# Performance work log

Hardware: AMD Instinct MI355X
Metric: run time of the kernel (lower is better)

The kernel has to match this reference:

```python
import jax, jax.numpy as jnp
import numpy as np

B, T, D, H = 4, 2048, 1024, 16
DH = D // H          # 64
HALF = DH // 2       # 32


def _rope_tables(T, half, base=10000.0):
    inv_freq = 1.0 / (base ** (np.arange(half, dtype=np.float32) / half))
    t = np.arange(T, dtype=np.float32)
    ang = np.outer(t, inv_freq)                       # [T, half]
    cos = jnp.asarray(np.cos(ang))[None, None]        # [1,1,T,half]
    sin = jnp.asarray(np.sin(ang))[None, None]
    return cos, sin


def setup_inputs() -> dict:
    key = jax.random.key(0)
    kx, kq, kp = jax.random.split(key, 3)
    cos, sin = _rope_tables(T, HALF)
    return {
        "x": jax.random.normal(kx, (B, T, D), dtype=jnp.float32),
        "cos": cos,
        "sin": sin,
        "W_qkv": jax.random.normal(kq, (3 * D, D), dtype=jnp.float32) * (D ** -0.5),
        "W_proj": jax.random.normal(kp, (D, D), dtype=jnp.float32) * (D ** -0.5),
    }


def _apply_rope(q, k, cos, sin):
    # q,k: [B,H,T,dh]; cos,sin: [1,1,T,dh/2]
    t = q.shape[2]
    c, s = cos[:, :, :t, :], sin[:, :, :t, :]
    h = q.shape[-1] // 2
    q1, q2 = q[..., :h], q[..., h:]
    k1, k2 = k[..., :h], k[..., h:]
    q_rot = jnp.concatenate([q1 * c - q2 * s, q1 * s + q2 * c], axis=-1)
    k_rot = jnp.concatenate([k1 * c - k2 * s, k1 * s + k2 * c], axis=-1)
    return q_rot, k_rot


def reference(x, cos, sin, W_qkv, W_proj):
    Bb, Tt, C = x.shape
    qkv = x @ W_qkv.T                                 # [B,T,3C]
    q, k, v = jnp.split(qkv, 3, axis=2)
    # [B,T,C] -> [B,H,T,dh]
    q = q.reshape(Bb, Tt, H, DH).transpose(0, 2, 1, 3)
    k = k.reshape(Bb, Tt, H, DH).transpose(0, 2, 1, 3)
    v = v.reshape(Bb, Tt, H, DH).transpose(0, 2, 1, 3)
    q, k = _apply_rope(q, k, cos, sin)
    w = jnp.einsum("bhqd,bhkd->bhqk", q, k) * (DH ** -0.5)
    causal = jnp.tril(jnp.ones((Tt, Tt), dtype=bool))
    w = jnp.where(causal, w, -jnp.inf)
    w = jax.nn.softmax(w.astype(jnp.float32), axis=-1).astype(x.dtype)
    out = jnp.einsum("bhqk,bhkd->bhqd", w, v)
    # XSA: subtract self-value contribution (diagonal attention weight)
    self_w = jnp.diagonal(w, axis1=-2, axis2=-1)[..., None]  # [B,H,T,1]
    out = out - self_w * v
    out = out.transpose(0, 2, 1, 3).reshape(Bb, Tt, C)
    return out @ W_proj.T
```

## Files before the change

kernel.cpp:

```cpp
#include <hip/hip_runtime.h>

constexpr int Tq = 2048;
constexpr int Dq = 1024;

typedef __bf16 bf16x8 __attribute__((ext_vector_type(8)));
typedef float f32x4 __attribute__((ext_vector_type(4)));
typedef _Float16 f16;
typedef f16 f16x4 __attribute__((ext_vector_type(4)));
typedef unsigned short u16;
typedef u16 u16x4 __attribute__((ext_vector_type(4)));
typedef u16 u16x8 __attribute__((ext_vector_type(8)));

__device__ __forceinline__ u16 f2bf(float f) {
    unsigned int u = __float_as_uint(f);
    u += 0x7fffu + ((u >> 16) & 1u);
    return (u16)(u >> 16);
}

__device__ __forceinline__ void gld_lds16(const void* g, void* l) {
    __builtin_amdgcn_global_load_lds(
        (const __attribute__((address_space(1))) unsigned int*)g,
        (__attribute__((address_space(3))) unsigned int*)l, 16, 0, 0);
}

__global__ void cvt3_f32_bf16(const float* __restrict__ a, u16* __restrict__ oa, int na,
                              const float* __restrict__ b, u16* __restrict__ ob, int nb,
                              const float* __restrict__ c, u16* __restrict__ oc, int nc) {
    int i = blockIdx.x * 256 + threadIdx.x;
    const float* in; u16* out;
    if (i < na) { in = a; out = oa; }
    else if (i < na + nb) { in = b; out = ob; i -= na; }
    else if (i < na + nb + nc) { in = c; out = oc; i -= na + nb; }
    else return;
    float4 v = ((const float4*)in)[i];
    u16x4 o;
    o.x = f2bf(v.x); o.y = f2bf(v.y); o.z = f2bf(v.z); o.w = f2bf(v.w);
    ((u16x4*)out)[i] = o;
}

__global__ __launch_bounds__(256) void gemm_qkv(const u16* __restrict__ A,
                                                const u16* __restrict__ B,
                                                const float* __restrict__ cosT,
                                                const float* __restrict__ sinT,
                                                u16* __restrict__ Qb,
                                                u16* __restrict__ Kb,
                                                f16* __restrict__ Vtg) {
    constexpr int K = 1024, N = 3072;
    __shared__ u16 As[128 * 32];
    __shared__ u16 Bs[128 * 32];
    const int t = threadIdx.x;
    const int lane = t & 63;
    const int wave = t >> 6;
    const int l16 = lane & 15;
    const int quad = lane >> 4;
    const int bm = blockIdx.x * 128;
    const int by = blockIdx.y;
    const int bn = by * 128;
    const int wm = (wave & 1) * 64;
    const int wn = (wave >> 1) * 64;
    const int srow = t >> 2;
    const int scol = (t & 3) * 8;

    f32x4 acc[4][4] = {};

    const u16* Ab = A + (size_t)(bm + srow) * K + scol;
    const u16* Bb = B + (size_t)(bn + srow) * K + scol;

    for (int k0 = 0; k0 < K; k0 += 32) {
        gld_lds16(Ab + k0,                    (char*)As + t * 16);
        gld_lds16(Ab + (size_t)64 * K + k0,   (char*)As + 4096 + t * 16);
        gld_lds16(Bb + k0,                    (char*)Bs + t * 16);
        gld_lds16(Bb + (size_t)64 * K + k0,   (char*)Bs + 4096 + t * 16);
        __syncthreads();

        bf16x8 af[4], bf[4];
#pragma unroll
        for (int i = 0; i < 4; i++) {
            af[i] = *(const bf16x8*)&As[(wm + i * 16 + l16) * 32 + quad * 8];
            bf[i] = *(const bf16x8*)&Bs[(wn + i * 16 + l16) * 32 + quad * 8];
        }
#pragma unroll
        for (int i = 0; i < 4; i++)
#pragma unroll
            for (int j = 0; j < 4; j++)
                acc[i][j] = __builtin_amdgcn_mfma_f32_16x16x32_bf16(af[i], bf[j], acc[i][j], 0, 0, 0);
        __syncthreads();
    }

    const int kind = by >> 3;
    if (kind < 2) {
        u16* Out = kind ? Kb : Qb;
        const float qscale = kind ? 1.f : 0.18033688011112042f;
        const int h = ((by & 7) << 1) + (wn >> 6);
#pragma unroll
        for (int i = 0; i < 4; i++)
#pragma unroll
            for (int r = 0; r < 4; r++) {
                const int gm = bm + wm + i * 16 + quad * 4 + r;
                const int b = gm >> 11, tt = gm & 2047;
                const size_t row = ((size_t)(b * 16 + h) * Tq + tt) * 64;
#pragma unroll
                for (int jj = 0; jj < 2; jj++) {
                    const int dd = jj * 16 + l16;
                    const float c = cosT[tt * 32 + dd];
                    const float s = sinT[tt * 32 + dd];
                    const float v1 = acc[i][jj][r];
                    const float v2 = acc[i][jj + 2][r];
                    Out[row + dd]      = f2bf((v1 * c - v2 * s) * qscale);
                    Out[row + dd + 32] = f2bf((v1 * s + v2 * c) * qscale);
                }
            }
    } else {
#pragma unroll
        for (int i = 0; i < 4; i++) {
            const int gm0 = bm + wm + i * 16 + quad * 4;
            const int b = gm0 >> 11, tt = gm0 & 2047;
#pragma unroll
            for (int j = 0; j < 4; j++) {
                const int col = wn + j * 16 + l16;
                const int h = ((by & 7) << 1) + (col >> 6);
                const int d = col & 63;
                f16x4 o = {(f16)acc[i][j][0], (f16)acc[i][j][1],
                           (f16)acc[i][j][2], (f16)acc[i][j][3]};
                *(f16x4*)&Vtg[((size_t)(b * 16 + h) * 64 + d) * Tq + tt] = o;
            }
        }
    }
}

__global__ __launch_bounds__(256) void gemm_bt(const u16* __restrict__ A,
                                               const u16* __restrict__ B,
                                               float* __restrict__ Cv,
                                               int M, int N, int K) {
    __shared__ u16 As[128 * 32];
    __shared__ u16 Bs[128 * 32];
    const int t = threadIdx.x;
    const int lane = t & 63;
    const int wave = t >> 6;
    const int l16 = lane & 15;
    const int quad = lane >> 4;
    const int bm = blockIdx.x * 128;
    const int bn = blockIdx.y * 128;
    const int wm = (wave & 1) * 64;
    const int wn = (wave >> 1) * 64;
    const int srow = t >> 2;
    const int scol = (t & 3) * 8;

    f32x4 acc[4][4] = {};

    const u16* Ab = A + (size_t)(bm + srow) * K + scol;
    const u16* Bb = B + (size_t)(bn + srow) * K + scol;

    for (int k0 = 0; k0 < K; k0 += 32) {
        gld_lds16(Ab + k0,                    (char*)As + t * 16);
        gld_lds16(Ab + (size_t)64 * K + k0,   (char*)As + 4096 + t * 16);
        gld_lds16(Bb + k0,                    (char*)Bs + t * 16);
        gld_lds16(Bb + (size_t)64 * K + k0,   (char*)Bs + 4096 + t * 16);
        __syncthreads();

        bf16x8 af[4], bf[4];
#pragma unroll
        for (int i = 0; i < 4; i++) {
            af[i] = *(const bf16x8*)&As[(wm + i * 16 + l16) * 32 + quad * 8];
            bf[i] = *(const bf16x8*)&Bs[(wn + i * 16 + l16) * 32 + quad * 8];
        }
#pragma unroll
        for (int i = 0; i < 4; i++)
#pragma unroll
            for (int j = 0; j < 4; j++)
                acc[i][j] = __builtin_amdgcn_mfma_f32_16x16x32_bf16(af[i], bf[j], acc[i][j], 0, 0, 0);
        __syncthreads();
    }

#pragma unroll
    for (int i = 0; i < 4; i++)
#pragma unroll
        for (int j = 0; j < 4; j++)
#pragma unroll
            for (int r = 0; r < 4; r++) {
                const int gm = bm + wm + i * 16 + quad * 4 + r;
                const int gn = bn + wn + j * 16 + l16;
                Cv[(size_t)gm * N + gn] = acc[i][j][r];
            }
}

template <bool MASK>
__device__ __forceinline__ void flash_tile(const u16* __restrict__ Ks,
                                           const f16* __restrict__ Vs,
                                           const bf16x8& qf0, const bf16x8& qf1,
                                           int l16, int quad, int i_loc,
                                           float& l_run, f32x4* o_acc) {
    f32x4 s[4];
    const int cp0 = quad ^ (l16 & 7);
    const int cp1 = (4 + quad) ^ (l16 & 7);
    __builtin_amdgcn_s_setprio(1);
#pragma unroll
    for (int tn = 0; tn < 4; tn++) {
        const int jrow = tn * 16 + l16;
        bf16x8 kf0 = *(const bf16x8*)&Ks[jrow * 64 + cp0 * 8];
        bf16x8 kf1 = *(const bf16x8*)&Ks[jrow * 64 + cp1 * 8];
        f32x4 z = {0.f, 0.f, 0.f, 0.f};
        z = __builtin_amdgcn_mfma_f32_16x16x32_bf16(kf0, qf0, z, 0, 0, 0);
        z = __builtin_amdgcn_mfma_f32_16x16x32_bf16(kf1, qf1, z, 0, 0, 0);
        s[tn] = z;
    }
    __builtin_amdgcn_s_setprio(0);
    float rsa[4];
#pragma unroll
    for (int tn = 0; tn < 4; tn++) {
        float rs = 0.f;
#pragma unroll
        for (int r = 0; r < 4; r++) {
            float v = s[tn][r];
            if (MASK) {
                const int j_loc = tn * 16 + quad * 4 + r;
                if (j_loc > i_loc) v = -1e30f;
            }
            float p = exp2f(v);
            rs += p;
            if (MASK) {
                const int j_loc = tn * 16 + quad * 4 + r;
                if (j_loc == i_loc) p = 0.f;
            }
            s[tn][r] = p;
        }
        rsa[tn] = rs;
    }
    l_run += (rsa[0] + rsa[1]) + (rsa[2] + rsa[3]);

    f16x4 pf[4];
#pragma unroll
    for (int tk = 0; tk < 4; tk++)
        pf[tk] = f16x4{(f16)s[tk][0], (f16)s[tk][1], (f16)s[tk][2], (f16)s[tk][3]};
    __builtin_amdgcn_s_setprio(1);
#pragma unroll
    for (int td = 0; td < 4; td++) {
        const int drow = td * 16 + l16;
#pragma unroll
        for (int tk = 0; tk < 4; tk++) {
            const int cp = (2 * tk + (quad >> 1)) ^ (l16 & 7);
            f16x4 vf = *(const f16x4*)&Vs[drow * 64 + cp * 8 + (quad & 1) * 4];
            o_acc[td] = __builtin_amdgcn_mfma_f32_16x16x16f16(vf, pf[tk], o_acc[td], 0, 0, 0);
        }
    }
    __builtin_amdgcn_s_setprio(0);
}

template <bool MASKA>
__device__ __forceinline__ void flash_tile2(const u16* __restrict__ Ks,
                                            const f16* __restrict__ Vs,
                                            const bf16x8& qa0, const bf16x8& qa1,
                                            const bf16x8& qb0, const bf16x8& qb1,
                                            int l16, int quad, int i_loc,
                                            float& lA, f32x4* oA,
                                            float& lB, f32x4* oB) {
    f32x4 sA[4], sB[4];
    const int cp0 = quad ^ (l16 & 7);
    const int cp1 = (4 + quad) ^ (l16 & 7);
    __builtin_amdgcn_s_setprio(1);
#pragma unroll
    for (int tn = 0; tn < 4; tn++) {
        const int jrow = tn * 16 + l16;
        bf16x8 kf0 = *(const bf16x8*)&Ks[jrow * 64 + cp0 * 8];
        bf16x8 kf1 = *(const bf16x8*)&Ks[jrow * 64 + cp1 * 8];
        f32x4 zA = {0.f, 0.f, 0.f, 0.f}, zB = {0.f, 0.f, 0.f, 0.f};
        zA = __builtin_amdgcn_mfma_f32_16x16x32_bf16(kf0, qa0, zA, 0, 0, 0);
        zB = __builtin_amdgcn_mfma_f32_16x16x32_bf16(kf0, qb0, zB, 0, 0, 0);
        zA = __builtin_amdgcn_mfma_f32_16x16x32_bf16(kf1, qa1, zA, 0, 0, 0);
        zB = __builtin_amdgcn_mfma_f32_16x16x32_bf16(kf1, qb1, zB, 0, 0, 0);
        sA[tn] = zA; sB[tn] = zB;
    }
    __builtin_amdgcn_s_setprio(0);
    float raA = 0.f, raB = 0.f;
#pragma unroll
    for (int tn = 0; tn < 4; tn++) {
#pragma unroll
        for (int r = 0; r < 4; r++) {
            float vA = sA[tn][r];
            if (MASKA) {
                const int j_loc = tn * 16 + quad * 4 + r;
                if (j_loc > i_loc) vA = -1e30f;
            }
            float pA = exp2f(vA);
            raA += pA;
            if (MASKA) {
                const int j_loc = tn * 16 + quad * 4 + r;
                if (j_loc == i_loc) pA = 0.f;
            }
            sA[tn][r] = pA;
            float pB = exp2f(sB[tn][r]);
            raB += pB;
            sB[tn][r] = pB;
        }
    }
    lA += raA; lB += raB;

    f16x4 pfA[4], pfB[4];
#pragma unroll
    for (int tk = 0; tk < 4; tk++) {
        pfA[tk] = f16x4{(f16)sA[tk][0], (f16)sA[tk][1], (f16)sA[tk][2], (f16)sA[tk][3]};
        pfB[tk] = f16x4{(f16)sB[tk][0], (f16)sB[tk][1], (f16)sB[tk][2], (f16)sB[tk][3]};
    }
    __builtin_amdgcn_s_setprio(1);
#pragma unroll
    for (int td = 0; td < 4; td++) {
        const int drow = td * 16 + l16;
#pragma unroll
        for (int tk = 0; tk < 4; tk++) {
            const int cp = (2 * tk + (quad >> 1)) ^ (l16 & 7);
            f16x4 vf = *(const f16x4*)&Vs[drow * 64 + cp * 8 + (quad & 1) * 4];
            oA[td] = __builtin_amdgcn_mfma_f32_16x16x16f16(vf, pfA[tk], oA[td], 0, 0, 0);
            oB[td] = __builtin_amdgcn_mfma_f32_16x16x16f16(vf, pfB[tk], oB[td], 0, 0, 0);
        }
    }
    __builtin_amdgcn_s_setprio(0);
}

__global__ __launch_bounds__(256, 2) void flash(const u16* __restrict__ Qb,
                                                const u16* __restrict__ Kb,
                                                const f16* __restrict__ Vtg,
                                                u16* __restrict__ Ob) {
    __shared__ __align__(16) char smem[65536];

    const int t = threadIdx.x, lane = t & 63, wave = t >> 6;
    const int l16 = lane & 15, quad = lane >> 4;
    const int i = blockIdx.x;
    const int xcd = i & 7, w = i >> 3;
    const int bh = xcd * 8 + (w >> 4);
    const int b = bh >> 4, h = bh & 15;
    const int x = w & 15;
    const int qtA = x, qtB = 31 - x;
    const int q0a = qtA * 64, q0b = qtB * 64;
    const u16* Qp = Qb + (size_t)bh * Tq * 64;
    const u16* Kp = Kb + (size_t)bh * Tq * 64;
    const f16* Vp = Vtg + (size_t)bh * 64 * Tq;

    const int rowi = wave * 16 + l16;
    bf16x8 qa0 = *(const bf16x8*)(Qp + (size_t)(q0a + rowi) * 64 + quad * 8);
    bf16x8 qa1 = *(const bf16x8*)(Qp + (size_t)(q0a + rowi) * 64 + 32 + quad * 8);
    bf16x8 qb0 = *(const bf16x8*)(Qp + (size_t)(q0b + rowi) * 64 + quad * 8);
    bf16x8 qb1 = *(const bf16x8*)(Qp + (size_t)(q0b + rowi) * 64 + 32 + quad * 8);
    asm volatile("s_waitcnt vmcnt(0)"
                 : "+v"(qa0), "+v"(qa1), "+v"(qb0), "+v"(qb1) :: "memory");

    float lA = 0.f, lB = 0.f;
    f32x4 oA[4] = {}, oB[4] = {};

    const int sr = t >> 3;
    const int sc = (t & 7) ^ (sr & 7);
    const int i_tloc = wave * 16 + l16;
    const int nt = 32 - x;
    const int nt2 = (nt + 1) >> 1;

    auto stage = [&](int n2) {
        const int j0 = n2 * 128;
        char* buf = smem + (n2 & 1) * 32768;
        gld_lds16(Kp + (size_t)(j0 + sr) * 64 + sc * 8,            buf + t * 16);
        gld_lds16(Kp + (size_t)(j0 + 32 + sr) * 64 + sc * 8,       buf + 4096 + t * 16);
        gld_lds16(Kp + (size_t)(j0 + 64 + sr) * 64 + sc * 8,       buf + 8192 + t * 16);
        gld_lds16(Kp + (size_t)(j0 + 96 + sr) * 64 + sc * 8,       buf + 12288 + t * 16);
        gld_lds16(Vp + (size_t)sr * Tq + j0 + sc * 8,              buf + 16384 + t * 16);
        gld_lds16(Vp + (size_t)(32 + sr) * Tq + j0 + sc * 8,       buf + 20480 + t * 16);
        gld_lds16(Vp + (size_t)sr * Tq + j0 + 64 + sc * 8,         buf + 24576 + t * 16);
        gld_lds16(Vp + (size_t)(32 + sr) * Tq + j0 + 64 + sc * 8,  buf + 28672 + t * 16);
    };

    stage(0);
    for (int n2 = 0; n2 < nt2; n2++) {
        asm volatile("s_waitcnt vmcnt(0)\n\ts_barrier" ::: "memory");
        if (n2 + 1 < nt2) stage(n2 + 1);
        char* cb = smem + (n2 & 1) * 32768;
#pragma unroll
        for (int s = 0; s < 2; s++) {
            const int tile = n2 * 2 + s;
            const u16* Ks = (const u16*)(cb + s * 8192);
            const f16* Vs = (const f16*)(cb + 16384 + s * 8192);
            if (tile < qtA)
                flash_tile2<false>(Ks, Vs, qa0, qa1, qb0, qb1, l16, quad, i_tloc,
                                   lA, oA, lB, oB);
            else if (tile == qtA)
                flash_tile2<true>(Ks, Vs, qa0, qa1, qb0, qb1, l16, quad, i_tloc,
                                  lA, oA, lB, oB);
            else if (tile < qtB)
                flash_tile<false>(Ks, Vs, qb0, qb1, l16, quad, i_tloc, lB, oB);
            else if (tile == qtB)
                flash_tile<true>(Ks, Vs, qb0, qb1, l16, quad, i_tloc, lB, oB);
        }
    }

    lA += __shfl_xor(lA, 16, 64);
    lA += __shfl_xor(lA, 32, 64);
    lB += __shfl_xor(lB, 16, 64);
    lB += __shfl_xor(lB, 32, 64);
    const float ivA = 1.f / lA, ivB = 1.f / lB;

    __syncthreads();
    u16* Os = (u16*)smem;
#pragma unroll
    for (int td = 0; td < 4; td++) {
        u16x4 oa, ob;
#pragma unroll
        for (int r = 0; r < 4; r++) {
            oa[r] = f2bf(oA[td][r] * ivA);
            ob[r] = f2bf(oB[td][r] * ivB);
        }
        *(u16x4*)&Os[wave * 1152 + l16 * 72 + td * 16 + quad * 4] = oa;
        *(u16x4*)&Os[(4 + wave) * 1152 + l16 * 72 + td * 16 + quad * 4] = ob;
    }
    __syncthreads();
    const int oi = lane >> 2, od = (lane & 3) * 16;
    {
        u16x8 r0 = *(const u16x8*)&Os[wave * 1152 + oi * 72 + od];
        u16x8 r1 = *(const u16x8*)&Os[wave * 1152 + oi * 72 + od + 8];
        const size_t orow = ((size_t)b * Tq + q0a + wave * 16 + oi) * Dq + h * 64 + od;
        *(u16x8*)&Ob[orow] = r0;
        *(u16x8*)&Ob[orow + 8] = r1;
    }
    {
        u16x8 r0 = *(const u16x8*)&Os[(4 + wave) * 1152 + oi * 72 + od];
        u16x8 r1 = *(const u16x8*)&Os[(4 + wave) * 1152 + oi * 72 + od + 8];
        const size_t orow = ((size_t)b * Tq + q0b + wave * 16 + oi) * Dq + h * 64 + od;
        *(u16x8*)&Ob[orow] = r0;
        *(u16x8*)&Ob[orow + 8] = r1;
    }
}

extern "C" void kernel_launch(void* const* d_in, const int* in_sizes, int n_in,
                              void* d_out, int out_size, void* d_ws, size_t ws_size,
                              hipStream_t stream) {
    const float* x     = (const float*)d_in[0];
    const float* cosT  = (const float*)d_in[1];
    const float* sinT  = (const float*)d_in[2];
    const float* Wqkv  = (const float*)d_in[3];
    const float* Wproj = (const float*)d_in[4];

    u16* xb     = (u16*)d_ws;
    u16* wqkvb  = xb + (size_t)8192 * 1024;
    u16* wprojb = wqkvb + (size_t)3072 * 1024;
    u16* Qb     = wprojb + (size_t)1024 * 1024;
    u16* Kb     = Qb + (size_t)64 * 2048 * 64;
    f16* Vtg    = (f16*)(Kb + (size_t)64 * 2048 * 64);
    u16* attn   = (u16*)(Vtg + (size_t)64 * 64 * 2048);

    cvt3_f32_bf16<<<12288, 256, 0, stream>>>(x, xb, 2097152,
                                             Wqkv, wqkvb, 786432,
                                             Wproj, wprojb, 262144);

    gemm_qkv<<<dim3(64, 24), 256, 0, stream>>>(xb, wqkvb, cosT, sinT, Qb, Kb, Vtg);
    flash<<<1024, 256, 0, stream>>>(Qb, Kb, Vtg, attn);
    gemm_bt<<<dim3(64, 8), 256, 0, stream>>>(attn, wprojb, (float*)d_out, 8192, 1024, 1024);
}
```

Measured before the change: 262.5 us.

## Compute softmax row sums via MFMA with ones matrix; grid-stride convert kernel

Result: no change. 262.1 us (-0.2%).

```diff
diff --git a/kernel.cpp b/kernel.cpp
--- a/kernel.cpp
+++ b/kernel.cpp
@@ -26,16 +26,17 @@
 __global__ void cvt3_f32_bf16(const float* __restrict__ a, u16* __restrict__ oa, int na,
                               const float* __restrict__ b, u16* __restrict__ ob, int nb,
                               const float* __restrict__ c, u16* __restrict__ oc, int nc) {
-    int i = blockIdx.x * 256 + threadIdx.x;
-    const float* in; u16* out;
-    if (i < na) { in = a; out = oa; }
-    else if (i < na + nb) { in = b; out = ob; i -= na; }
-    else if (i < na + nb + nc) { in = c; out = oc; i -= na + nb; }
-    else return;
-    float4 v = ((const float4*)in)[i];
-    u16x4 o;
-    o.x = f2bf(v.x); o.y = f2bf(v.y); o.z = f2bf(v.z); o.w = f2bf(v.w);
-    ((u16x4*)out)[i] = o;
+    const int ntot = na + nb + nc;
+    for (int i = blockIdx.x * 256 + threadIdx.x; i < ntot; i += 2048 * 256) {
+        const float* in; u16* out; int j = i;
+        if (j < na) { in = a; out = oa; }
+        else if (j < na + nb) { in = b; out = ob; j -= na; }
+        else { in = c; out = oc; j -= na + nb; }
+        float4 v = ((const float4*)in)[j];
+        u16x4 o;
+        o.x = f2bf(v.x); o.y = f2bf(v.y); o.z = f2bf(v.z); o.w = f2bf(v.w);
+        ((u16x4*)out)[j] = o;
+    }
 }
 
 __global__ __launch_bounds__(256) void gemm_qkv(const u16* __restrict__ A,
@@ -189,7 +190,7 @@
                                            const f16* __restrict__ Vs,
                                            const bf16x8& qf0, const bf16x8& qf1,
                                            int l16, int quad, int i_loc,
-                                           float& l_run, f32x4* o_acc) {
+                                           float& l_sc, f32x4& o_l, f32x4* o_acc) {
     f32x4 s[4];
     const int cp0 = quad ^ (l16 & 7);
     const int cp1 = (4 + quad) ^ (l16 & 7);
@@ -205,34 +206,40 @@
         s[tn] = z;
     }
     __builtin_amdgcn_s_setprio(0);
-    float rsa[4];
-#pragma unroll
-    for (int tn = 0; tn < 4; tn++) {
-        float rs = 0.f;
-#pragma unroll
-        for (int r = 0; r < 4; r++) {
-            float v = s[tn][r];
-            if (MASK) {
+    if (MASK) {
+        float rsa = 0.f;
+#pragma unroll
+        for (int tn = 0; tn < 4; tn++)
+#pragma unroll
+            for (int r = 0; r < 4; r++) {
                 const int j_loc = tn * 16 + quad * 4 + r;
+                float v = s[tn][r];
                 if (j_loc > i_loc) v = -1e30f;
-            }
-            float p = exp2f(v);
-            rs += p;
-            if (MASK) {
-                const int j_loc = tn * 16 + quad * 4 + r;
+                float p = exp2f(v);
+                rsa += p;
                 if (j_loc == i_loc) p = 0.f;
-            }
-            s[tn][r] = p;
-        }
-        rsa[tn] = rs;
-    }
-    l_run += (rsa[0] + rsa[1]) + (rsa[2] + rsa[3]);
+                s[tn][r] = p;
+            }
+        l_sc += rsa;
+    } else {
+#pragma unroll
+        for (int tn = 0; tn < 4; tn++)
+#pragma unroll
+            for (int r = 0; r < 4; r++)
+                s[tn][r] = exp2f(s[tn][r]);
+    }
 
     f16x4 pf[4];
 #pragma unroll
     for (int tk = 0; tk < 4; tk++)
         pf[tk] = f16x4{(f16)s[tk][0], (f16)s[tk][1], (f16)s[tk][2], (f16)s[tk][3]};
     __builtin_amdgcn_s_setprio(1);
+    if (!MASK) {
+        const f16x4 ones = {(f16)1.f, (f16)1.f, (f16)1.f, (f16)1.f};
+#pragma unroll
+        for (int tk = 0; tk < 4; tk++)
+            o_l = __builtin_amdgcn_mfma_f32_16x16x16f16(ones, pf[tk], o_l, 0, 0, 0);
+    }
 #pragma unroll
     for (int td = 0; td < 4; td++) {
         const int drow = td * 16 + l16;
@@ -252,8 +259,8 @@
                                             const bf16x8& qa0, const bf16x8& qa1,
                                             const bf16x8& qb0, const bf16x8& qb1,
                                             int l16, int quad, int i_loc,
-                                            float& lA, f32x4* oA,
-                                            float& lB, f32x4* oB) {
+                                            float& lA_sc, f32x4& olA, f32x4* oA,
+                                            f32x4& olB, f32x4* oB) {
     f32x4 sA[4], sB[4];
     const int cp0 = quad ^ (l16 & 7);
     const int cp1 = (4 + quad) ^ (l16 & 7);
@@ -271,29 +278,31 @@
         sA[tn] = zA; sB[tn] = zB;
     }
     __builtin_amdgcn_s_setprio(0);
-    float raA = 0.f, raB = 0.f;
-#pragma unroll
-    for (int tn = 0; tn < 4; tn++) {
-#pragma unroll
-        for (int r = 0; r < 4; r++) {
-            float vA = sA[tn][r];
-            if (MASKA) {
+    if (MASKA) {
+        float rsa = 0.f;
+#pragma unroll
+        for (int tn = 0; tn < 4; tn++)
+#pragma unroll
+            for (int r = 0; r < 4; r++) {
                 const int j_loc = tn * 16 + quad * 4 + r;
+                float vA = sA[tn][r];
                 if (j_loc > i_loc) vA = -1e30f;
-            }
-            float pA = exp2f(vA);
-            raA += pA;
-            if (MASKA) {
-                const int j_loc = tn * 16 + quad * 4 + r;
+                float pA = exp2f(vA);
+                rsa += pA;
                 if (j_loc == i_loc) pA = 0.f;
-            }
-            sA[tn][r] = pA;
-            float pB = exp2f(sB[tn][r]);
-            raB += pB;
-            sB[tn][r] = pB;
-        }
-    }
-    lA += raA; lB += raB;
+                sA[tn][r] = pA;
+                sB[tn][r] = exp2f(sB[tn][r]);
+            }
+        lA_sc += rsa;
+    } else {
+#pragma unroll
+        for (int tn = 0; tn < 4; tn++)
+#pragma unroll
+            for (int r = 0; r < 4; r++) {
+                sA[tn][r] = exp2f(sA[tn][r]);
+                sB[tn][r] = exp2f(sB[tn][r]);
+            }
+    }
 
     f16x4 pfA[4], pfB[4];
 #pragma unroll
@@ -302,6 +311,15 @@
         pfB[tk] = f16x4{(f16)sB[tk][0], (f16)sB[tk][1], (f16)sB[tk][2], (f16)sB[tk][3]};
     }
     __builtin_amdgcn_s_setprio(1);
+    {
+        const f16x4 ones = {(f16)1.f, (f16)1.f, (f16)1.f, (f16)1.f};
+#pragma unroll
+        for (int tk = 0; tk < 4; tk++) {
+            if (!MASKA)
+                olA = __builtin_amdgcn_mfma_f32_16x16x16f16(ones, pfA[tk], olA, 0, 0, 0);
+            olB = __builtin_amdgcn_mfma_f32_16x16x16f16(ones, pfB[tk], olB, 0, 0, 0);
+        }
+    }
 #pragma unroll
     for (int td = 0; td < 4; td++) {
         const int drow = td * 16 + l16;
@@ -343,7 +361,8 @@
     asm volatile("s_waitcnt vmcnt(0)"
                  : "+v"(qa0), "+v"(qa1), "+v"(qb0), "+v"(qb1) :: "memory");
 
-    float lA = 0.f, lB = 0.f;
+    float lA_sc = 0.f;
+    f32x4 olA = {}, olB = {};
     f32x4 oA[4] = {}, oB[4] = {};
 
     const int sr = t >> 3;
@@ -377,22 +396,27 @@
             const f16* Vs = (const f16*)(cb + 16384 + s * 8192);
             if (tile < qtA)
                 flash_tile2<false>(Ks, Vs, qa0, qa1, qb0, qb1, l16, quad, i_tloc,
-                                   lA, oA, lB, oB);
+                                   lA_sc, olA, oA, olB, oB);
             else if (tile == qtA)
                 flash_tile2<true>(Ks, Vs, qa0, qa1, qb0, qb1, l16, quad, i_tloc,
-                                  lA, oA, lB, oB);
+                                  lA_sc, olA, oA, olB, oB);
             else if (tile < qtB)
-                flash_tile<false>(Ks, Vs, qb0, qb1, l16, quad, i_tloc, lB, oB);
-            else if (tile == qtB)
-                flash_tile<true>(Ks, Vs, qb0, qb1, l16, quad, i_tloc, lB, oB);
-        }
-    }
-
-    lA += __shfl_xor(lA, 16, 64);
-    lA += __shfl_xor(lA, 32, 64);
-    lB += __shfl_xor(lB, 16, 64);
-    lB += __shfl_xor(lB, 32, 64);
-    const float ivA = 1.f / lA, ivB = 1.f / lB;
+                flash_tile<false>(Ks, Vs, qb0, qb1, l16, quad, i_tloc, lA_sc, olB, oB);
+            else if (tile == qtB) {
+                float lB_sc = 0.f;
+                f32x4 dummy = {};
+                flash_tile<true>(Ks, Vs, qb0, qb1, l16, quad, i_tloc, lB_sc, dummy, oB);
+                lB_sc += __shfl_xor(lB_sc, 16, 64);
+                lB_sc += __shfl_xor(lB_sc, 32, 64);
+                olB[0] += lB_sc;
+            }
+        }
+    }
+
+    lA_sc += __shfl_xor(lA_sc, 16, 64);
+    lA_sc += __shfl_xor(lA_sc, 32, 64);
+    const float ivA = 1.f / (olA[0] + lA_sc);
+    const float ivB = 1.f / olB[0];
 
     __syncthreads();
     u16* Os = (u16*)smem;
@@ -442,9 +466,9 @@
     f16* Vtg    = (f16*)(Kb + (size_t)64 * 2048 * 64);
     u16* attn   = (u16*)(Vtg + (size_t)64 * 64 * 2048);
 
-    cvt3_f32_bf16<<<12288, 256, 0, stream>>>(x, xb, 2097152,
-                                             Wqkv, wqkvb, 786432,
-                                             Wproj, wprojb, 262144);
+    cvt3_f32_bf16<<<2048, 256, 0, stream>>>(x, xb, 2097152,
+                                            Wqkv, wqkvb, 786432,
+                                            Wproj, wprojb, 262144);
 
     gemm_qkv<<<dim3(64, 24), 256, 0, stream>>>(xb, wqkvb, cosT, sinT, Qb, Kb, Vtg);
     flash<<<1024, 256, 0, stream>>>(Qb, Kb, Vtg, attn);
```
